# Kernel tuning notes

Measured on AMD Instinct MI355X. Metric: run time of the kernel, lower is better.

Reference implementation:

```python
import jax, jax.numpy as jnp
import numpy as np

_GROUP_SIZES = [4096, 2048, 1024, 8192, 512, 3072, 6144, 1024]
_K = 2048
_N = 2048


def setup_inputs() -> dict:
    key = jax.random.key(0)
    keys = jax.random.split(key, len(_GROUP_SIZES) + 1)
    inp = {}
    for i, m in enumerate(_GROUP_SIZES):
        inp[f"A{i}"] = jax.random.normal(keys[i], (m, _K), dtype=jnp.float32)
    inp["B_shared"] = jax.random.normal(keys[-1], (_K, _N), dtype=jnp.float32)
    return inp


def reference(A0, A1, A2, A3, A4, A5, A6, A7, B_shared):
    # torch: cat([a @ B for a in group_A], dim=0)
    # Concatenating ragged groups first and doing one GEMM is the same math
    # (row-block structure of matmul), expressed as a single fused contraction.
    A_cat = jnp.concatenate([A0, A1, A2, A3, A4, A5, A6, A7], axis=0)  # [M_total, K]
    return A_cat @ B_shared  # [M_total, N]
```

## Files before the change

kernel.cpp:

```cpp
#include <hip/hip_runtime.h>
#include <hip/hip_bf16.h>

using short8  = __attribute__((ext_vector_type(8))) short;
using ushort8 = __attribute__((ext_vector_type(8))) unsigned short;
using f32x4   = __attribute__((ext_vector_type(4))) float;

#define GLB(p)  ((const __attribute__((address_space(1))) void*)(p))
#define LDSP(p) ((__attribute__((address_space(3))) void*)(p))

static __device__ __forceinline__ unsigned short f2bf(float f) {
    union { float f; unsigned u; } v; v.f = f;
    unsigned u = v.u;
    u += 0x7fffu + ((u >> 16) & 1u);
    return (unsigned short)(u >> 16);
}

#define K_DIM 2048
#define N_DIM 2048
#define M_TOTAL 26112
#define N_GROUPS 8

__global__ __launch_bounds__(256) void cvt_a_all(
        const float* __restrict__ A0, const float* __restrict__ A1,
        const float* __restrict__ A2, const float* __restrict__ A3,
        const float* __restrict__ A4, const float* __restrict__ A5,
        const float* __restrict__ A6, const float* __restrict__ A7,
        unsigned short* __restrict__ Acat) {
    int b = blockIdx.x;
    const float* src; int gb;
    if      (b < 256)  { src = A0; gb = 0;    }
    else if (b < 384)  { src = A1; gb = 256;  }
    else if (b < 448)  { src = A2; gb = 384;  }
    else if (b < 960)  { src = A3; gb = 448;  }
    else if (b < 992)  { src = A4; gb = 960;  }
    else if (b < 1184) { src = A5; gb = 992;  }
    else if (b < 1568) { src = A6; gb = 1184; }
    else               { src = A7; gb = 1568; }
    const float* s    = src  + (long)(b - gb) * 16 * K_DIM;
    unsigned short* d = Acat + (long)b * 16 * K_DIM;
    int t = threadIdx.x;
#pragma unroll 4
    for (int i = 0; i < 16; ++i) {
        long off = (long)i * K_DIM + t * 8;
        float4 x = *(const float4*)(s + off);
        float4 y = *(const float4*)(s + off + 4);
        ushort8 o;
        o[0] = f2bf(x.x); o[1] = f2bf(x.y); o[2] = f2bf(x.z); o[3] = f2bf(x.w);
        o[4] = f2bf(y.x); o[5] = f2bf(y.y); o[6] = f2bf(y.z); o[7] = f2bf(y.w);
        *(ushort8*)(d + off) = o;
    }
}

__global__ __launch_bounds__(256) void cvt_bt_kernel(const float* __restrict__ B,
                                                     unsigned short* __restrict__ Bt) {
    __shared__ float t[32][33];
    int bx = blockIdx.x, by = blockIdx.y;
    int tx = threadIdx.x, ty = threadIdx.y;
#pragma unroll
    for (int i = 0; i < 32; i += 8)
        t[ty + i][tx] = B[(long)(by * 32 + ty + i) * N_DIM + bx * 32 + tx];
    __syncthreads();
#pragma unroll
    for (int i = 0; i < 32; i += 8)
        Bt[(long)(bx * 32 + ty + i) * K_DIM + by * 32 + tx] = f2bf(t[tx][ty + i]);
}


#define PBAR() __builtin_amdgcn_s_barrier()
#define VMC(n)  asm volatile("s_waitcnt vmcnt(" #n ")" ::: "memory")

#define ST_A(BUF, H, L, TT)                                                        \
    __builtin_amdgcn_global_load_lds(                                              \
        GLB(aSt + (long)((H) * 128 + (L) * 64) * K_DIM + (TT) * 64),               \
        LDSP(lds + (BUF) * 32768 + (H) * 8192 + (L) * 4096 + w * 512), 16, 0, 0)
#define ST_B(BUF, H, L, TT)                                                        \
    __builtin_amdgcn_global_load_lds(                                              \
        GLB(bSt + (long)((H) * 128 + (L) * 64) * K_DIM + (TT) * 64),               \
        LDSP(lds + (BUF) * 32768 + 16384 + (H) * 8192 + (L) * 4096 + w * 512), 16, 0, 0)

#define MMQ(MH, NH, AV, BV)                                                        \
    _Pragma("unroll") for (int i = 0; i < 4; ++i)                                  \
    _Pragma("unroll") for (int j = 0; j < 2; ++j)                                  \
        acc[(MH) * 4 + i][(NH) * 2 + j] = __builtin_amdgcn_mfma_f32_16x16x32_bf16( \
            AV[i], BV[j], acc[(MH) * 4 + i][(NH) * 2 + j], 0, 0, 0);

#define TILE(BUF, T, DO1, DO2)                                                          \
    do {                                                                                \
        const unsigned short* pA = lds + (BUF) * 32768 + wm * 1024 + r16 * 64;          \
        const unsigned short* pB = lds + (BUF) * 32768 + 16384 + wn * 1024 + r16 * 64;  \
        short8 a0[4], a1[4], b00[2], b01[2], b10[2], b11[2];                            \
                        \
        _Pragma("unroll") for (int i = 0; i < 4; ++i) {                                 \
            a0[i] = *(const short8*)(pA + i * 2048 + c0 * 8);                           \
            a1[i] = *(const short8*)(pA + i * 2048 + c1 * 8);                           \
        }                                                                               \
        _Pragma("unroll") for (int j = 0; j < 2; ++j) {                                 \
            b00[j] = *(const short8*)(pB + j * 4096 + c0 * 8);                          \
            b01[j] = *(const short8*)(pB + j * 4096 + c1 * 8);                          \
        }                                                                               \
        if (DO1) { ST_A((BUF) ^ 1, 1, 0, (T) + 1); ST_A((BUF) ^ 1, 1, 1, (T) + 1); }    \
        PBAR();                                                                         \
        __builtin_amdgcn_s_setprio(1); MMQ(0, 0, a0, b00); MMQ(0, 0, a1, b01);          \
        __builtin_amdgcn_s_setprio(0); PBAR();                                          \
                                 \
        _Pragma("unroll") for (int j = 0; j < 2; ++j) {                                 \
            b10[j] = *(const short8*)(pB + 8192 + j * 4096 + c0 * 8);                   \
            b11[j] = *(const short8*)(pB + 8192 + j * 4096 + c1 * 8);                   \
        }                                                                               \
        if (DO2) { ST_A((BUF), 0, 0, (T) + 2); ST_A((BUF), 0, 1, (T) + 2); }            \
        PBAR();                                                                         \
        __builtin_amdgcn_s_setprio(1); MMQ(0, 1, a0, b10); MMQ(0, 1, a1, b11);          \
        __builtin_amdgcn_s_setprio(0); PBAR();                                          \
                                 \
        _Pragma("unroll") for (int i = 0; i < 4; ++i) {                                 \
            a0[i] = *(const short8*)(pA + 8192 + i * 2048 + c0 * 8);                    \
            a1[i] = *(const short8*)(pA + 8192 + i * 2048 + c1 * 8);                    \
        }                                                                               \
        if (DO2) { ST_B((BUF), 0, 0, (T) + 2); ST_B((BUF), 0, 1, (T) + 2); }            \
        PBAR();                                                                         \
        __builtin_amdgcn_s_setprio(1); MMQ(1, 0, a0, b00); MMQ(1, 0, a1, b01);          \
        __builtin_amdgcn_s_setprio(0); PBAR();                                          \
                             \
        if (DO2) { ST_B((BUF), 1, 0, (T) + 2); ST_B((BUF), 1, 1, (T) + 2); }            \
        __builtin_amdgcn_s_setprio(1); MMQ(1, 1, a0, b10); MMQ(1, 1, a1, b11);          \
        __builtin_amdgcn_s_setprio(0);                                                  \
    } while (0)

#define ST_A4(BUF, TT)                                                             \
    __builtin_amdgcn_global_load_lds(                                              \
        GLB(aSt + (long)(TT) * 64),                                                \
        LDSP(lds + (BUF) * 4096 + w * 512), 16, 0, 0)
#define ST_B4(BUF, H, L, TT)                                                       \
    __builtin_amdgcn_global_load_lds(                                              \
        GLB(bSt + (long)((H) * 128 + (L) * 64) * K_DIM + (TT) * 64),               \
        LDSP(lds + 8192 + (BUF) * 16384 + (H) * 8192 + (L) * 4096 + w * 512), 16, 0, 0)

#define MMQ4(NH, AV, BV)                                                           \
    _Pragma("unroll") for (int i = 0; i < 2; ++i)                                  \
    _Pragma("unroll") for (int j = 0; j < 2; ++j)                                  \
        acc[i][(NH) * 2 + j] = __builtin_amdgcn_mfma_f32_16x16x32_bf16(            \
            AV[i], BV[j], acc[i][(NH) * 2 + j], 0, 0, 0);

#define TILE64(BUF, T, DO2)                                                             \
    do {                                                                                \
        const unsigned short* pA = lds + (BUF) * 4096 + wm * 1024 + r16 * 64;           \
        const unsigned short* pB = lds + 8192 + (BUF) * 16384 + wn * 1024 + r16 * 64;   \
        short8 a0[2], a1[2], b00[2], b01[2], b10[2], b11[2];                            \
              \
        _Pragma("unroll") for (int i = 0; i < 2; ++i) {                                 \
            a0[i] = *(const short8*)(pA + i * 2048 + c0 * 8);                           \
            a1[i] = *(const short8*)(pA + i * 2048 + c1 * 8);                           \
        }                                                                               \
        _Pragma("unroll") for (int j = 0; j < 2; ++j) {                                 \
            b00[j] = *(const short8*)(pB + j * 4096 + c0 * 8);                          \
            b01[j] = *(const short8*)(pB + j * 4096 + c1 * 8);                          \
        }                                                                               \
        PBAR();                                                                         \
        __builtin_amdgcn_s_setprio(1); MMQ4(0, a0, b00);                                \
        __builtin_amdgcn_s_setprio(0); PBAR();                                          \
                                 \
        _Pragma("unroll") for (int j = 0; j < 2; ++j) {                                 \
            b10[j] = *(const short8*)(pB + 8192 + j * 4096 + c0 * 8);                   \
            b11[j] = *(const short8*)(pB + 8192 + j * 4096 + c1 * 8);                   \
        }                                                                               \
        PBAR();                                                                         \
        __builtin_amdgcn_s_setprio(1); MMQ4(0, a1, b01);                                \
        __builtin_amdgcn_s_setprio(0); PBAR();                                          \
                                          \
        if (DO2) { ST_B4((BUF), 0, 0, (T) + 2); ST_B4((BUF), 0, 1, (T) + 2); }          \
        PBAR();                                                                         \
        __builtin_amdgcn_s_setprio(1); MMQ4(1, a0, b10);                                \
        __builtin_amdgcn_s_setprio(0); PBAR();                                          \
                                 \
        if (DO2) { ST_B4((BUF), 1, 0, (T) + 2); ST_B4((BUF), 1, 1, (T) + 2);            \
                   ST_A4((BUF), (T) + 2); }                                             \
        __builtin_amdgcn_s_setprio(1); MMQ4(1, a1, b11);                                \
        __builtin_amdgcn_s_setprio(0);                                                  \
    } while (0)

__global__ __launch_bounds__(512, 2) void gemm8_kernel(const unsigned short* __restrict__ Acat,
                                                       const unsigned short* __restrict__ Bt,
                                                       float* __restrict__ C) {
    __shared__ unsigned short lds[65536];

    int wg  = blockIdx.x;
    int tid = threadIdx.x;
    int l   = tid & 63;
    int w   = tid >> 6;
    int wm  = w >> 2;
    int wn  = w & 3;
    int r16 = l & 15, kq = l >> 4, x = l & 7;
    int c0  = kq ^ x;
    int c1  = (4 + kq) ^ x;
    int srow = tid >> 3;
    int sq   = (tid & 7) ^ (srow & 7);

    if (wg < 768) {
        int swz = (wg & 7) * 102 + (wg >> 3);
        int mt  = swz >> 3, nt = swz & 7;
        int m0  = mt * 256, n0 = nt * 256;

        const unsigned short* aSt = Acat + (long)(m0 + srow) * K_DIM + sq * 8;
        const unsigned short* bSt = Bt   + (long)(n0 + srow) * K_DIM + sq * 8;

        f32x4 acc[8][4] = {};

        ST_A(0, 0, 0, 0); ST_A(0, 0, 1, 0); ST_A(0, 1, 0, 0); ST_A(0, 1, 1, 0);
        ST_B(0, 0, 0, 0); ST_B(0, 0, 1, 0); ST_B(0, 1, 0, 0); ST_B(0, 1, 1, 0);
        ST_A(1, 0, 0, 1); ST_A(1, 0, 1, 1);
        ST_B(1, 0, 0, 1); ST_B(1, 0, 1, 1); ST_B(1, 1, 0, 1); ST_B(1, 1, 1, 1);
        VMC(6); PBAR();

#pragma unroll 1
        for (int t = 0; t < 30; t += 2) {
            TILE(0, t, 1, 1);     VMC(6); PBAR();
            TILE(1, t + 1, 1, 1); VMC(6); PBAR();
        }
        TILE(0, 30, 1, 0); VMC(0); PBAR();
        TILE(1, 31, 0, 0);

        int orow = m0 + wm * 16 + (l >> 4) * 4;
        int ocol = n0 + wn * 16 + (l & 15);
#pragma unroll
        for (int i = 0; i < 8; ++i)
#pragma unroll
            for (int j = 0; j < 4; ++j)
#pragma unroll
                for (int q = 0; q < 4; ++q)
                    C[(long)(orow + i * 32 + q) * N_DIM + (ocol + j * 64)] = acc[i][j][q];
    } else {
        int k    = wg - 768;
        int o    = 768 + (k >> 2);
        int qh   = k & 3;
        int swz  = (o & 7) * 102 + (o >> 3);
        int mt   = swz >> 3, nt = swz & 7;
        int m0   = mt * 256 + qh * 64, n0 = nt * 256;

        const unsigned short* aSt = Acat + (long)(m0 + srow) * K_DIM + sq * 8;
        const unsigned short* bSt = Bt   + (long)(n0 + srow) * K_DIM + sq * 8;

        f32x4 acc[2][4] = {};

        ST_A4(0, 0);
        ST_B4(0, 0, 0, 0); ST_B4(0, 0, 1, 0); ST_B4(0, 1, 0, 0); ST_B4(0, 1, 1, 0);
        ST_A4(1, 1);
        ST_B4(1, 0, 0, 1); ST_B4(1, 0, 1, 1); ST_B4(1, 1, 0, 1); ST_B4(1, 1, 1, 1);
        VMC(5); PBAR();

#pragma unroll 1
        for (int t = 0; t < 30; ++t) {
            TILE64(t & 1, t, 1); VMC(5); PBAR();
        }
        TILE64(0, 30, 0); VMC(0); PBAR();
        TILE64(1, 31, 0);

        int orow = m0 + wm * 16 + (l >> 4) * 4;
        int ocol = n0 + wn * 16 + (l & 15);
#pragma unroll
        for (int i = 0; i < 2; ++i)
#pragma unroll
            for (int j = 0; j < 4; ++j)
#pragma unroll
                for (int q = 0; q < 4; ++q)
                    C[(long)(orow + i * 32 + q) * N_DIM + (ocol + j * 64)] = acc[i][j][q];
    }
}

__global__ void naive_gemm_kernel(const float* __restrict__ A, const float* __restrict__ B,
                                  float* __restrict__ C, int M) {
    __shared__ float As[16][16];
    __shared__ float Bs[16][17];
    int tx = threadIdx.x, ty = threadIdx.y;
    int row = blockIdx.y * 16 + ty;
    int col = blockIdx.x * 16 + tx;
    float s = 0.f;
    for (int k0 = 0; k0 < K_DIM; k0 += 16) {
        As[ty][tx] = A[(long)row * K_DIM + k0 + tx];
        Bs[ty][tx] = B[(long)(k0 + ty) * N_DIM + col];
        __syncthreads();
#pragma unroll
        for (int t = 0; t < 16; ++t) s += As[ty][t] * Bs[t][tx];
        __syncthreads();
    }
    C[(long)row * N_DIM + col] = s;
}

extern "C" void kernel_launch(void* const* d_in, const int* in_sizes, int n_in,
                              void* d_out, int out_size, void* d_ws, size_t ws_size,
                              hipStream_t stream) {
    static const int g_m[N_GROUPS]   = {4096, 2048, 1024, 8192, 512, 3072, 6144, 1024};
    static const int g_off[N_GROUPS] = {0, 4096, 6144, 7168, 15360, 15872, 18944, 25088};

    float* C = (float*)d_out;
    const size_t need = ((size_t)M_TOTAL * K_DIM + (size_t)N_DIM * K_DIM) * 2;

    if (ws_size >= need) {
        unsigned short* Acat = (unsigned short*)d_ws;
        unsigned short* Bt   = Acat + (size_t)M_TOTAL * K_DIM;

        cvt_a_all<<<M_TOTAL / 16, 256, 0, stream>>>(
            (const float*)d_in[0], (const float*)d_in[1], (const float*)d_in[2],
            (const float*)d_in[3], (const float*)d_in[4], (const float*)d_in[5],
            (const float*)d_in[6], (const float*)d_in[7], Acat);
        cvt_bt_kernel<<<dim3(N_DIM / 32, K_DIM / 32), dim3(32, 8), 0, stream>>>(
            (const float*)d_in[8], Bt);

        gemm8_kernel<<<768 + 192, 512, 0, stream>>>(Acat, Bt, C);
    } else {
        for (int g = 0; g < N_GROUPS; ++g)
            naive_gemm_kernel<<<dim3(N_DIM / 16, g_m[g] / 16), dim3(16, 16), 0, stream>>>(
                (const float*)d_in[g], (const float*)d_in[8], C + (size_t)g_off[g] * N_DIM,
                g_m[g]);
    }
}
```

Before: 280.9 us.

## Fuse fp32-to-bf16 A conversion into GEMM register-staged loads

Removes the separate pass that converts and concatenates all A groups to bf16. The GEMM now selects the group pointer per tile, loads fp32 A into registers two tiles ahead, converts to bf16 and writes it into swizzled LDS after the MFMA phase. This drops a full read/write pass over A (about 200 MB of traffic) and a kernel launch. In exchange each tile reads twice as many A bytes from global memory, and the register-staged pipeline uses more VGPRs and adds waitcnt synchronisation inside the main loop.

```diff
diff --git a/kernel.cpp b/kernel.cpp
--- a/kernel.cpp
+++ b/kernel.cpp
@@ -3,6 +3,7 @@
 
 using short8  = __attribute__((ext_vector_type(8))) short;
 using ushort8 = __attribute__((ext_vector_type(8))) unsigned short;
+using us4     = __attribute__((ext_vector_type(4))) unsigned short;
 using f32x4   = __attribute__((ext_vector_type(4))) float;
 
 #define GLB(p)  ((const __attribute__((address_space(1))) void*)(p))
@@ -14,42 +15,14 @@
     u += 0x7fffu + ((u >> 16) & 1u);
     return (unsigned short)(u >> 16);
 }
+static __device__ __forceinline__ unsigned short f2bfc(float f) {
+    return __builtin_bit_cast(unsigned short, __float2bfloat16(f));
+}
 
 #define K_DIM 2048
 #define N_DIM 2048
 #define M_TOTAL 26112
 #define N_GROUPS 8
-
-__global__ __launch_bounds__(256) void cvt_a_all(
-        const float* __restrict__ A0, const float* __restrict__ A1,
-        const float* __restrict__ A2, const float* __restrict__ A3,
-        const float* __restrict__ A4, const float* __restrict__ A5,
-        const float* __restrict__ A6, const float* __restrict__ A7,
-        unsigned short* __restrict__ Acat) {
-    int b = blockIdx.x;
-    const float* src; int gb;
-    if      (b < 256)  { src = A0; gb = 0;    }
-    else if (b < 384)  { src = A1; gb = 256;  }
-    else if (b < 448)  { src = A2; gb = 384;  }
-    else if (b < 960)  { src = A3; gb = 448;  }
-    else if (b < 992)  { src = A4; gb = 960;  }
-    else if (b < 1184) { src = A5; gb = 992;  }
-    else if (b < 1568) { src = A6; gb = 1184; }
-    else               { src = A7; gb = 1568; }
-    const float* s    = src  + (long)(b - gb) * 16 * K_DIM;
-    unsigned short* d = Acat + (long)b * 16 * K_DIM;
-    int t = threadIdx.x;
-#pragma unroll 4
-    for (int i = 0; i < 16; ++i) {
-        long off = (long)i * K_DIM + t * 8;
-        float4 x = *(const float4*)(s + off);
-        float4 y = *(const float4*)(s + off + 4);
-        ushort8 o;
-        o[0] = f2bf(x.x); o[1] = f2bf(x.y); o[2] = f2bf(x.z); o[3] = f2bf(x.w);
-        o[4] = f2bf(y.x); o[5] = f2bf(y.y); o[6] = f2bf(y.z); o[7] = f2bf(y.w);
-        *(ushort8*)(d + off) = o;
-    }
-}
 
 __global__ __launch_bounds__(256) void cvt_bt_kernel(const float* __restrict__ B,
                                                      unsigned short* __restrict__ Bt) {
@@ -66,13 +39,11 @@
 }
 
 
-#define PBAR() __builtin_amdgcn_s_barrier()
+#define PBAR()  __builtin_amdgcn_s_barrier()
+#define LGKM0() asm volatile("s_waitcnt lgkmcnt(0)" ::: "memory")
 #define VMC(n)  asm volatile("s_waitcnt vmcnt(" #n ")" ::: "memory")
-
-#define ST_A(BUF, H, L, TT)                                                        \
-    __builtin_amdgcn_global_load_lds(                                              \
-        GLB(aSt + (long)((H) * 128 + (L) * 64) * K_DIM + (TT) * 64),               \
-        LDSP(lds + (BUF) * 32768 + (H) * 8192 + (L) * 4096 + w * 512), 16, 0, 0)
+#define SBAR0() __builtin_amdgcn_sched_barrier(0)
+
 #define ST_B(BUF, H, L, TT)                                                        \
     __builtin_amdgcn_global_load_lds(                                              \
         GLB(bSt + (long)((H) * 128 + (L) * 64) * K_DIM + (TT) * 64),               \
@@ -84,12 +55,24 @@
         acc[(MH) * 4 + i][(NH) * 2 + j] = __builtin_amdgcn_mfma_f32_16x16x32_bf16( \
             AV[i], BV[j], acc[(MH) * 4 + i][(NH) * 2 + j], 0, 0, 0);
 
-#define TILE(BUF, T, DO1, DO2)                                                          \
+#define ALD(AR, N_I, T2)                                                           \
+    do { _Pragma("unroll") for (int i = 0; i < (N_I); ++i)                         \
+            AR[i] = *(const float4*)(aB + (long)(i * 32) * K_DIM + (T2) * 64);     \
+        SBAR0(); } while (0)
+
+#define AWRN(BASE, AR, N_I)                                                        \
+    do { _Pragma("unroll") for (int i = 0; i < (N_I); ++i) {                       \
+        us4 o = { f2bfc(AR[i].x), f2bfc(AR[i].y), f2bfc(AR[i].z), f2bfc(AR[i].w) };\
+        *(us4*)(lds + (BASE) + (ar0 + i * 32) * 64 + awch * 8 + wsub) = o;         \
+    } } while (0)
+
+#define TILE(BUF, T, DOA, DOB)                                                          \
     do {                                                                                \
         const unsigned short* pA = lds + (BUF) * 32768 + wm * 1024 + r16 * 64;          \
         const unsigned short* pB = lds + (BUF) * 32768 + 16384 + wn * 1024 + r16 * 64;  \
         short8 a0[4], a1[4], b00[2], b01[2], b10[2], b11[2];                            \
-                        \
+        float4 ar[8];                                                                   \
+                         \
         _Pragma("unroll") for (int i = 0; i < 4; ++i) {                                 \
             a0[i] = *(const short8*)(pA + i * 2048 + c0 * 8);                           \
             a1[i] = *(const short8*)(pA + i * 2048 + c1 * 8);                           \
@@ -98,38 +81,34 @@
             b00[j] = *(const short8*)(pB + j * 4096 + c0 * 8);                          \
             b01[j] = *(const short8*)(pB + j * 4096 + c1 * 8);                          \
         }                                                                               \
-        if (DO1) { ST_A((BUF) ^ 1, 1, 0, (T) + 1); ST_A((BUF) ^ 1, 1, 1, (T) + 1); }    \
+        if (DOA) ALD(ar, 8, (T) + 2);                                                   \
         PBAR();                                                                         \
         __builtin_amdgcn_s_setprio(1); MMQ(0, 0, a0, b00); MMQ(0, 0, a1, b01);          \
         __builtin_amdgcn_s_setprio(0); PBAR();                                          \
-                                 \
+                                                         \
         _Pragma("unroll") for (int j = 0; j < 2; ++j) {                                 \
             b10[j] = *(const short8*)(pB + 8192 + j * 4096 + c0 * 8);                   \
             b11[j] = *(const short8*)(pB + 8192 + j * 4096 + c1 * 8);                   \
         }                                                                               \
-        if (DO2) { ST_A((BUF), 0, 0, (T) + 2); ST_A((BUF), 0, 1, (T) + 2); }            \
         PBAR();                                                                         \
         __builtin_amdgcn_s_setprio(1); MMQ(0, 1, a0, b10); MMQ(0, 1, a1, b11);          \
         __builtin_amdgcn_s_setprio(0); PBAR();                                          \
-                                 \
+                                        \
         _Pragma("unroll") for (int i = 0; i < 4; ++i) {                                 \
             a0[i] = *(const short8*)(pA + 8192 + i * 2048 + c0 * 8);                    \
             a1[i] = *(const short8*)(pA + 8192 + i * 2048 + c1 * 8);                    \
         }                                                                               \
-        if (DO2) { ST_B((BUF), 0, 0, (T) + 2); ST_B((BUF), 0, 1, (T) + 2); }            \
+        if (DOB) { ST_B((BUF), 0, 0, (T) + 2); ST_B((BUF), 0, 1, (T) + 2); }            \
         PBAR();                                                                         \
         __builtin_amdgcn_s_setprio(1); MMQ(1, 0, a0, b00); MMQ(1, 0, a1, b01);          \
         __builtin_amdgcn_s_setprio(0); PBAR();                                          \
-                             \
-        if (DO2) { ST_B((BUF), 1, 0, (T) + 2); ST_B((BUF), 1, 1, (T) + 2); }            \
+             \
+        if (DOB) { ST_B((BUF), 1, 0, (T) + 2); ST_B((BUF), 1, 1, (T) + 2); }            \
         __builtin_amdgcn_s_setprio(1); MMQ(1, 1, a0, b10); MMQ(1, 1, a1, b11);          \
         __builtin_amdgcn_s_setprio(0);                                                  \
+        if (DOA) { VMC(4); SBAR0(); AWRN((BUF) * 32768, ar, 8); }                       \
     } while (0)
 
-#define ST_A4(BUF, TT)                                                             \
-    __builtin_amdgcn_global_load_lds(                                              \
-        GLB(aSt + (long)(TT) * 64),                                                \
-        LDSP(lds + (BUF) * 4096 + w * 512), 16, 0, 0)
 #define ST_B4(BUF, H, L, TT)                                                       \
     __builtin_amdgcn_global_load_lds(                                              \
         GLB(bSt + (long)((H) * 128 + (L) * 64) * K_DIM + (TT) * 64),               \
@@ -141,12 +120,13 @@
         acc[i][(NH) * 2 + j] = __builtin_amdgcn_mfma_f32_16x16x32_bf16(            \
             AV[i], BV[j], acc[i][(NH) * 2 + j], 0, 0, 0);
 
-#define TILE64(BUF, T, DO2)                                                             \
+#define TILE64(BUF, T, DOA, DOB)                                                        \
     do {                                                                                \
         const unsigned short* pA = lds + (BUF) * 4096 + wm * 1024 + r16 * 64;           \
         const unsigned short* pB = lds + 8192 + (BUF) * 16384 + wn * 1024 + r16 * 64;   \
         short8 a0[2], a1[2], b00[2], b01[2], b10[2], b11[2];                            \
-              \
+        float4 ar[2];                                                                   \
+                        \
         _Pragma("unroll") for (int i = 0; i < 2; ++i) {                                 \
             a0[i] = *(const short8*)(pA + i * 2048 + c0 * 8);                           \
             a1[i] = *(const short8*)(pA + i * 2048 + c1 * 8);                           \
@@ -155,10 +135,11 @@
             b00[j] = *(const short8*)(pB + j * 4096 + c0 * 8);                          \
             b01[j] = *(const short8*)(pB + j * 4096 + c1 * 8);                          \
         }                                                                               \
+        if (DOA) ALD(ar, 2, (T) + 2);                                                   \
         PBAR();                                                                         \
         __builtin_amdgcn_s_setprio(1); MMQ4(0, a0, b00);                                \
         __builtin_amdgcn_s_setprio(0); PBAR();                                          \
-                                 \
+                                                              \
         _Pragma("unroll") for (int j = 0; j < 2; ++j) {                                 \
             b10[j] = *(const short8*)(pB + 8192 + j * 4096 + c0 * 8);                   \
             b11[j] = *(const short8*)(pB + 8192 + j * 4096 + c1 * 8);                   \
@@ -166,21 +147,24 @@
         PBAR();                                                                         \
         __builtin_amdgcn_s_setprio(1); MMQ4(0, a1, b01);                                \
         __builtin_amdgcn_s_setprio(0); PBAR();                                          \
-                                          \
-        if (DO2) { ST_B4((BUF), 0, 0, (T) + 2); ST_B4((BUF), 0, 1, (T) + 2); }          \
+                                                        \
+        if (DOB) { ST_B4((BUF), 0, 0, (T) + 2); ST_B4((BUF), 0, 1, (T) + 2); }          \
         PBAR();                                                                         \
         __builtin_amdgcn_s_setprio(1); MMQ4(1, a0, b10);                                \
         __builtin_amdgcn_s_setprio(0); PBAR();                                          \
-                                 \
-        if (DO2) { ST_B4((BUF), 1, 0, (T) + 2); ST_B4((BUF), 1, 1, (T) + 2);            \
-                   ST_A4((BUF), (T) + 2); }                                             \
+                            \
+        if (DOB) { ST_B4((BUF), 1, 0, (T) + 2); ST_B4((BUF), 1, 1, (T) + 2); }          \
         __builtin_amdgcn_s_setprio(1); MMQ4(1, a1, b11);                                \
         __builtin_amdgcn_s_setprio(0);                                                  \
+        if (DOA) { VMC(4); SBAR0(); AWRN((BUF) * 4096, ar, 2); }                        \
     } while (0)
 
-__global__ __launch_bounds__(512, 2) void gemm8_kernel(const unsigned short* __restrict__ Acat,
-                                                       const unsigned short* __restrict__ Bt,
-                                                       float* __restrict__ C) {
+__global__ __launch_bounds__(512, 2) void gemm8_kernel(
+        const float* __restrict__ A0, const float* __restrict__ A1,
+        const float* __restrict__ A2, const float* __restrict__ A3,
+        const float* __restrict__ A4, const float* __restrict__ A5,
+        const float* __restrict__ A6, const float* __restrict__ A7,
+        const unsigned short* __restrict__ Bt, float* __restrict__ C) {
     __shared__ unsigned short lds[65536];
 
     int wg  = blockIdx.x;
@@ -195,28 +179,51 @@
     int srow = tid >> 3;
     int sq   = (tid & 7) ^ (srow & 7);
 
+    int c4   = l & 15;
+    int ar0  = w * 4 + (l >> 4);
+    int awch = (c4 >> 1) ^ (ar0 & 7);
+    int wsub = (c4 & 1) * 4;
+
     if (wg < 768) {
         int swz = (wg & 7) * 102 + (wg >> 3);
         int mt  = swz >> 3, nt = swz & 7;
         int m0  = mt * 256, n0 = nt * 256;
 
-        const unsigned short* aSt = Acat + (long)(m0 + srow) * K_DIM + sq * 8;
-        const unsigned short* bSt = Bt   + (long)(n0 + srow) * K_DIM + sq * 8;
+        const float* aBase; int goff;
+        if      (mt < 16) { aBase = A0; goff = 0;     }
+        else if (mt < 24) { aBase = A1; goff = 4096;  }
+        else if (mt < 28) { aBase = A2; goff = 6144;  }
+        else if (mt < 60) { aBase = A3; goff = 7168;  }
+        else if (mt < 62) { aBase = A4; goff = 15360; }
+        else if (mt < 74) { aBase = A5; goff = 15872; }
+        else if (mt < 98) { aBase = A6; goff = 18944; }
+        else              { aBase = A7; goff = 25088; }
+        const float* aB = aBase + (long)(m0 - goff + ar0) * K_DIM + c4 * 4;
+        const unsigned short* bSt = Bt + (long)(n0 + srow) * K_DIM + sq * 8;
 
         f32x4 acc[8][4] = {};
 
-        ST_A(0, 0, 0, 0); ST_A(0, 0, 1, 0); ST_A(0, 1, 0, 0); ST_A(0, 1, 1, 0);
-        ST_B(0, 0, 0, 0); ST_B(0, 0, 1, 0); ST_B(0, 1, 0, 0); ST_B(0, 1, 1, 0);
-        ST_A(1, 0, 0, 1); ST_A(1, 0, 1, 1);
-        ST_B(1, 0, 0, 1); ST_B(1, 0, 1, 1); ST_B(1, 1, 0, 1); ST_B(1, 1, 1, 1);
-        VMC(6); PBAR();
+        {
+            float4 arA[8], arB[8];
+#pragma unroll
+            for (int i = 0; i < 8; ++i) arA[i] = *(const float4*)(aB + (long)(i * 32) * K_DIM);
+#pragma unroll
+            for (int i = 0; i < 8; ++i) arB[i] = *(const float4*)(aB + (long)(i * 32) * K_DIM + 64);
+            SBAR0();
+            ST_B(0, 0, 0, 0); ST_B(0, 0, 1, 0); ST_B(0, 1, 0, 0); ST_B(0, 1, 1, 0);
+            ST_B(1, 0, 0, 1); ST_B(1, 0, 1, 1); ST_B(1, 1, 0, 1); ST_B(1, 1, 1, 1);
+            VMC(8); SBAR0();
+            AWRN(0, arA, 8);
+            AWRN(32768, arB, 8);
+            VMC(4); LGKM0(); PBAR();
+        }
 
 #pragma unroll 1
         for (int t = 0; t < 30; t += 2) {
-            TILE(0, t, 1, 1);     VMC(6); PBAR();
-            TILE(1, t + 1, 1, 1); VMC(6); PBAR();
+            TILE(0, t, 1, 1);     PBAR();
+            TILE(1, t + 1, 1, 1); PBAR();
         }
-        TILE(0, 30, 1, 0); VMC(0); PBAR();
+        TILE(0, 30, 0, 0); VMC(0); PBAR();
         TILE(1, 31, 0, 0);
 
         int orow = m0 + wm * 16 + (l >> 4) * 4;
@@ -236,23 +243,41 @@
         int mt   = swz >> 3, nt = swz & 7;
         int m0   = mt * 256 + qh * 64, n0 = nt * 256;
 
-        const unsigned short* aSt = Acat + (long)(m0 + srow) * K_DIM + sq * 8;
-        const unsigned short* bSt = Bt   + (long)(n0 + srow) * K_DIM + sq * 8;
+        const float* aBase; int goff;
+        if      (mt < 16) { aBase = A0; goff = 0;     }
+        else if (mt < 24) { aBase = A1; goff = 4096;  }
+        else if (mt < 28) { aBase = A2; goff = 6144;  }
+        else if (mt < 60) { aBase = A3; goff = 7168;  }
+        else if (mt < 62) { aBase = A4; goff = 15360; }
+        else if (mt < 74) { aBase = A5; goff = 15872; }
+        else if (mt < 98) { aBase = A6; goff = 18944; }
+        else              { aBase = A7; goff = 25088; }
+        const float* aB = aBase + (long)(m0 - goff + ar0) * K_DIM + c4 * 4;
+        const unsigned short* bSt = Bt + (long)(n0 + srow) * K_DIM + sq * 8;
 
         f32x4 acc[2][4] = {};
 
-        ST_A4(0, 0);
-        ST_B4(0, 0, 0, 0); ST_B4(0, 0, 1, 0); ST_B4(0, 1, 0, 0); ST_B4(0, 1, 1, 0);
-        ST_A4(1, 1);
-        ST_B4(1, 0, 0, 1); ST_B4(1, 0, 1, 1); ST_B4(1, 1, 0, 1); ST_B4(1, 1, 1, 1);
-        VMC(5); PBAR();
+        {
+            float4 arA[2], arB[2];
+#pragma unroll
+            for (int i = 0; i < 2; ++i) arA[i] = *(const float4*)(aB + (long)(i * 32) * K_DIM);
+#pragma unroll
+            for (int i = 0; i < 2; ++i) arB[i] = *(const float4*)(aB + (long)(i * 32) * K_DIM + 64);
+            SBAR0();
+            ST_B4(0, 0, 0, 0); ST_B4(0, 0, 1, 0); ST_B4(0, 1, 0, 0); ST_B4(0, 1, 1, 0);
+            ST_B4(1, 0, 0, 1); ST_B4(1, 0, 1, 1); ST_B4(1, 1, 0, 1); ST_B4(1, 1, 1, 1);
+            VMC(8); SBAR0();
+            AWRN(0, arA, 2);
+            AWRN(4096, arB, 2);
+            VMC(4); LGKM0(); PBAR();
+        }
 
 #pragma unroll 1
         for (int t = 0; t < 30; ++t) {
-            TILE64(t & 1, t, 1); VMC(5); PBAR();
+            TILE64(t & 1, t, 1, 1); PBAR();
         }
-        TILE64(0, 30, 0); VMC(0); PBAR();
-        TILE64(1, 31, 0);
+        TILE64(0, 30, 0, 0); VMC(0); PBAR();
+        TILE64(1, 31, 0, 0);
 
         int orow = m0 + wm * 16 + (l >> 4) * 4;
         int ocol = n0 + wn * 16 + (l & 15);
@@ -292,20 +317,16 @@
     static const int g_off[N_GROUPS] = {0, 4096, 6144, 7168, 15360, 15872, 18944, 25088};
 
     float* C = (float*)d_out;
-    const size_t need = ((size_t)M_TOTAL * K_DIM + (size_t)N_DIM * K_DIM) * 2;
+    const size_t need = (size_t)N_DIM * K_DIM * 2;
 
     if (ws_size >= need) {
-        unsigned short* Acat = (unsigned short*)d_ws;
-        unsigned short* Bt   = Acat + (size_t)M_TOTAL * K_DIM;
-
-        cvt_a_all<<<M_TOTAL / 16, 256, 0, stream>>>(
+        unsigned short* Bt = (unsigned short*)d_ws;
+        cvt_bt_kernel<<<dim3(N_DIM / 32, K_DIM / 32), dim3(32, 8), 0, stream>>>(
+            (const float*)d_in[8], Bt);
+        gemm8_kernel<<<768 + 192, 512, 0, stream>>>(
             (const float*)d_in[0], (const float*)d_in[1], (const float*)d_in[2],
             (const float*)d_in[3], (const float*)d_in[4], (const float*)d_in[5],
-            (const float*)d_in[6], (const float*)d_in[7], Acat);
-        cvt_bt_kernel<<<dim3(N_DIM / 32, K_DIM / 32), dim3(32, 8), 0, stream>>>(
-            (const float*)d_in[8], Bt);
-
-        gemm8_kernel<<<768 + 192, 512, 0, stream>>>(Acat, Bt, C);
+            (const float*)d_in[6], (const float*)d_in[7], Bt, C);
     } else {
         for (int g = 0; g < N_GROUPS; ++g)
             naive_gemm_kernel<<<dim3(N_DIM / 16, g_m[g] / 16), dim3(16, 16), 0, stream>>>(
```

Result: slower. 339.9 us (+21.0%).
